# Performance work log

Measured on AMD Instinct MI355X. Metric: run time of the kernel, lower is better.

## Reference

```python
import jax, jax.numpy as jnp
import numpy as np

CHUNK = 32  # chunk_size in delta_rule_chunkwise


def _l2norm(x):
    return x * jax.lax.rsqrt(jnp.sum(x * x, axis=-1, keepdims=True) + 1e-6)


def setup_inputs() -> dict:
    key = jax.random.key(0)
    kq, kk, kv, kb = jax.random.split(key, 4)
    b, h, L, d = 4, 4, 8192, 128
    q = jax.random.normal(kq, (b, h, L, d), dtype=jnp.float32)
    k = jax.random.normal(kk, (b, h, L, d), dtype=jnp.float32)
    v = jax.random.normal(kv, (b, h, L, d), dtype=jnp.float32)
    beta = jax.random.uniform(kb, (b, h, L), dtype=jnp.float32)  # sigmoid(b_proj) in (0,1)
    return {"q": q, "k": k, "v": v, "beta": beta}


def reference(q, k, v, beta):
    """Chunkwise DeltaNet delta-rule: strictly causal, O(N) in seq length.
    q,k: [b,h,L,dk]; v: [b,h,L,dv]; beta: [b,h,L]. L must be a multiple of CHUNK.
    Returns (o [b,h,L,dv], final state S [b,h,dk,dv])."""
    b, h, L, dk = q.shape
    dv = v.shape[-1]
    c = CHUNK
    n = L // c

    qn = _l2norm(q)
    kn = _l2norm(k)
    vb = v * beta[..., None]
    kb = kn * beta[..., None]

    resh = lambda t: t.reshape(b, h, n, c, t.shape[-1])  # b h (n c) d -> b h n c d
    qc, kc, vc, kbc = map(resh, (qn, kn, vb, kb))

    # A = -(k_beta @ k^T) with upper triangle (incl diag) zeroed
    upper_incl = jnp.triu(jnp.ones((c, c), dtype=bool), 0)
    A = jnp.where(upper_incl, 0.0, -(kbc @ jnp.swapaxes(kc, -1, -2)))  # [b,h,n,c,c]

    # sequential forward substitution: inv[i,:i] += inv[i,:] @ inv[:,:i]
    col = jnp.arange(c)

    def row_body(i, inv):
        row = inv[..., i, :]                                   # [b,h,n,c]
        upd = row + jnp.einsum('...j,...jk->...k', row, inv)   # row @ inv
        return inv.at[..., i, :].set(jnp.where(col < i, upd, row))

    inv = jax.lax.fori_loop(1, c, row_body, A)
    inv = inv + jnp.eye(c, dtype=inv.dtype)

    u = inv @ vc    # [b,h,n,c,dv]
    w = inv @ kbc   # [b,h,n,c,dk]

    strict_upper = jnp.triu(jnp.ones((c, c), dtype=bool), 1)

    def step(S, xs):
        q_i, k_i, u_i0, w_i = xs                                   # [b,h,c,*]
        attn = jnp.where(strict_upper, 0.0, q_i @ jnp.swapaxes(k_i, -1, -2))
        u_i = u_i0 - w_i @ S
        o_i = q_i @ S + attn @ u_i
        S = S + jnp.swapaxes(k_i, -1, -2) @ u_i
        return S, o_i

    xs = tuple(jnp.moveaxis(t, 2, 0) for t in (qc, kc, u, w))      # [n,b,h,c,*]
    S0 = jnp.zeros((b, h, dk, dv), dtype=q.dtype)
    S, o = jax.lax.scan(step, S0, xs)
    o = jnp.moveaxis(o, 0, 2).reshape(b, h, L, dv)
    return o, S
```

## Files before the change

### kernel.cpp

```cpp
#include <hip/hip_runtime.h>


static constexpr int BH   = 16;
static constexpr int LQ   = 8192;
static constexpr int DK   = 128;
static constexpr int CC   = 32;
static constexpr int NCH  = LQ / CC;
static constexpr int LDP  = 132;
static constexpr int TP   = 36;

static constexpr size_t W_OFF  = 0;
static constexpr size_t U0_OFF = (size_t)BH * NCH * CC * DK;
static constexpr size_t AT_OFF = U0_OFF * 2;
static constexpr size_t RQ_OFF = AT_OFF + (size_t)BH * NCH * CC * CC;
static constexpr size_t RK_OFF = RQ_OFF + (size_t)BH * LQ;

__global__ __launch_bounds__(256) void dn_phase1(
    const float* __restrict__ q, const float* __restrict__ k,
    const float* __restrict__ v, const float* __restrict__ beta,
    float* __restrict__ ws)
{
    __shared__ float qc[CC][LDP];
    __shared__ float kc[CC][LDP];
    __shared__ float vc[CC][LDP];
    __shared__ float T[CC][TP];
    __shared__ float betas[CC], rqs[CC], rks[CC];

    const int tid = threadIdx.x;
    const int blk = blockIdx.x;
    const int bh  = blk >> 8;
    const int t   = blk & 255;
    const size_t gbase = ((size_t)bh * LQ + (size_t)t * CC) * DK;

    #pragma unroll
    for (int i = 0; i < 4; ++i) {
        int idx4 = i * 256 + tid;
        int row  = idx4 >> 5;
        int c4   = (idx4 & 31) << 2;
        *(float4*)&qc[row][c4] = *(const float4*)(q + gbase + (size_t)idx4 * 4);
        *(float4*)&kc[row][c4] = *(const float4*)(k + gbase + (size_t)idx4 * 4);
        *(float4*)&vc[row][c4] = *(const float4*)(v + gbase + (size_t)idx4 * 4);
    }
    if (tid < CC) betas[tid] = beta[(size_t)bh * LQ + (size_t)t * CC + tid];
    __syncthreads();

    {
        int row = tid >> 3, g = tid & 7;
        float sq = 0.f, sk = 0.f;
        #pragma unroll
        for (int i = 0; i < 4; ++i) {
            float4 a = *(float4*)&qc[row][g * 16 + i * 4];
            sq += a.x * a.x + a.y * a.y + a.z * a.z + a.w * a.w;
            float4 b = *(float4*)&kc[row][g * 16 + i * 4];
            sk += b.x * b.x + b.y * b.y + b.z * b.z + b.w * b.w;
        }
        sq += __shfl_xor(sq, 1); sq += __shfl_xor(sq, 2); sq += __shfl_xor(sq, 4);
        sk += __shfl_xor(sk, 1); sk += __shfl_xor(sk, 2); sk += __shfl_xor(sk, 4);
        if (g == 0) {
            rqs[row] = 1.f / sqrtf(sq + 1e-6f);
            rks[row] = 1.f / sqrtf(sk + 1e-6f);
        }
    }
    __syncthreads();

    if (tid < CC) {
        ws[RQ_OFF + (size_t)bh * LQ + (size_t)t * CC + tid] = rqs[tid];
        ws[RK_OFF + (size_t)bh * LQ + (size_t)t * CC + tid] = rks[tid];
    }

    #pragma unroll
    for (int i = 0; i < 4; ++i) {
        int idx4 = i * 256 + tid;
        int row  = idx4 >> 5;
        int c4   = (idx4 & 31) << 2;
        float rq_ = rqs[row], rk_ = rks[row];
        float4 a = *(float4*)&qc[row][c4];
        a.x *= rq_; a.y *= rq_; a.z *= rq_; a.w *= rq_;
        *(float4*)&qc[row][c4] = a;
        float4 b = *(float4*)&kc[row][c4];
        b.x *= rk_; b.y *= rk_; b.z *= rk_; b.w *= rk_;
        *(float4*)&kc[row][c4] = b;
    }
    __syncthreads();

    {
        int i  = tid >> 3;
        int j0 = (tid & 7) << 2;
        float aA[4] = {0.f, 0.f, 0.f, 0.f};
        float aQ[4] = {0.f, 0.f, 0.f, 0.f};
        for (int r4 = 0; r4 < 32; ++r4) {
            float4 ki = *(float4*)&kc[i][r4 << 2];
            float4 qi = *(float4*)&qc[i][r4 << 2];
            #pragma unroll
            for (int jj = 0; jj < 4; ++jj) {
                float4 kj = *(float4*)&kc[j0 + jj][r4 << 2];
                aA[jj] += ki.x * kj.x + ki.y * kj.y + ki.z * kj.z + ki.w * kj.w;
                aQ[jj] += qi.x * kj.x + qi.y * kj.y + qi.z * kj.z + qi.w * kj.w;
            }
        }
        float bi = betas[i];
        float at4[4];
        #pragma unroll
        for (int jj = 0; jj < 4; ++jj) {
            int j = j0 + jj;
            T[i][j] = (j < i) ? (-bi * aA[jj]) : 0.f;
            at4[jj] = (j <= i) ? aQ[jj] : 0.f;
        }
        *(float4*)(ws + AT_OFF + ((size_t)(bh * NCH + t) * CC + i) * CC + j0) =
            make_float4(at4[0], at4[1], at4[2], at4[3]);
    }
    __syncthreads();

    for (int i = 1; i < CC; ++i) {
        float upd = 0.f;
        if (tid < i) {
            float s = T[i][tid];
            for (int j = 0; j < CC; ++j) s += T[i][j] * T[j][tid];
            upd = s;
        }
        __syncthreads();
        if (tid < i) T[i][tid] = upd;
        __syncthreads();
    }

    {
        int i  = tid >> 3;
        int j0 = (tid & 7) << 2;
        #pragma unroll
        for (int jj = 0; jj < 4; ++jj) T[i][j0 + jj] *= betas[j0 + jj];
    }
    __syncthreads();

    {
        int i  = tid >> 3;
        int d0 = (tid & 7) << 4;
        float bi = betas[i];
        float4 aU[4], aW[4];
        #pragma unroll
        for (int d4 = 0; d4 < 4; ++d4) {
            float4 vv = *(float4*)&vc[i][d0 + d4 * 4];
            float4 kk = *(float4*)&kc[i][d0 + d4 * 4];
            aU[d4] = make_float4(bi * vv.x, bi * vv.y, bi * vv.z, bi * vv.w);
            aW[d4] = make_float4(bi * kk.x, bi * kk.y, bi * kk.z, bi * kk.w);
        }
        for (int j = 0; j < i; ++j) {
            float tb = T[i][j];
            #pragma unroll
            for (int d4 = 0; d4 < 4; ++d4) {
                float4 vv = *(float4*)&vc[j][d0 + d4 * 4];
                float4 kk = *(float4*)&kc[j][d0 + d4 * 4];
                aU[d4].x += tb * vv.x; aU[d4].y += tb * vv.y;
                aU[d4].z += tb * vv.z; aU[d4].w += tb * vv.w;
                aW[d4].x += tb * kk.x; aW[d4].y += tb * kk.y;
                aW[d4].z += tb * kk.z; aW[d4].w += tb * kk.w;
            }
        }
        size_t ob = (size_t)(bh * NCH + t) * (CC * DK) + (size_t)i * DK + d0;
        #pragma unroll
        for (int d4 = 0; d4 < 4; ++d4) {
            *(float4*)(ws + U0_OFF + ob + d4 * 4) = aU[d4];
            *(float4*)(ws + W_OFF  + ob + d4 * 4) = aW[d4];
        }
    }
}

__global__ __launch_bounds__(256) void dn_phase2(
    const float* __restrict__ q, const float* __restrict__ k,
    const float* __restrict__ ws, float* __restrict__ out)
{
    __shared__ float wA[CC][LDP], kA[CC][LDP], qA[CC][LDP];
    __shared__ float wB[CC][LDP], kB[CC][LDP], qB[CC][LDP];
    __shared__ float aA_[CC][TP], aB_[CC][TP];
    __shared__ float St[8][LDP];
    __shared__ float um_[CC][12];
    __shared__ float u2_[CC][12];

    const int bh  = blockIdx.x >> 4;
    const int g   = blockIdx.x & 15;
    const int c0  = g * 8;
    const int tid = threadIdx.x;
    const int a   = tid >> 3;
    const int c   = tid & 7;
    const int k2  = tid & 127;
    const int ch  = tid >> 7;

    float sreg0 = 0.f, sreg1 = 0.f, sreg2 = 0.f, sreg3 = 0.f;

    for (int idx = tid; idx < 8 * LDP; idx += 256) ((float*)St)[idx] = 0.f;

    float4 sw0, sw1, sw2, sw3, sk0, sk1, sk2_, sk3, sq0, sq1, sq2, sq3, sat;
    float nu0, nrq, nrk;

    auto issue = [&](int t) {
        const size_t wb = W_OFF + (size_t)(bh * NCH + t) * 4096;
        const size_t gb = ((size_t)bh * LQ + (size_t)t * CC) * DK;
        const size_t ab = AT_OFF + (size_t)(bh * NCH + t) * 1024;
        sw0 = *(const float4*)(ws + wb + (size_t)(0 * 256 + tid) * 4);
        sw1 = *(const float4*)(ws + wb + (size_t)(1 * 256 + tid) * 4);
        sw2 = *(const float4*)(ws + wb + (size_t)(2 * 256 + tid) * 4);
        sw3 = *(const float4*)(ws + wb + (size_t)(3 * 256 + tid) * 4);
        sk0 = *(const float4*)(k + gb + (size_t)(0 * 256 + tid) * 4);
        sk1 = *(const float4*)(k + gb + (size_t)(1 * 256 + tid) * 4);
        sk2_ = *(const float4*)(k + gb + (size_t)(2 * 256 + tid) * 4);
        sk3 = *(const float4*)(k + gb + (size_t)(3 * 256 + tid) * 4);
        sq0 = *(const float4*)(q + gb + (size_t)(0 * 256 + tid) * 4);
        sq1 = *(const float4*)(q + gb + (size_t)(1 * 256 + tid) * 4);
        sq2 = *(const float4*)(q + gb + (size_t)(2 * 256 + tid) * 4);
        sq3 = *(const float4*)(q + gb + (size_t)(3 * 256 + tid) * 4);
        sat = *(const float4*)(ws + ab + (size_t)tid * 4);
        nu0 = ws[U0_OFF + (size_t)(bh * NCH + t) * 4096 + (size_t)a * DK + c0 + c];
        nrq = ws[RQ_OFF + (size_t)bh * LQ + (size_t)t * CC + a];
        nrk = ws[RK_OFF + (size_t)bh * LQ + (size_t)t * CC + a];
    };

    auto commit = [&](float (*wT)[LDP], float (*kT)[LDP], float (*qT)[LDP],
                      float (*aT)[TP]) {
        {
            int gi = 0 * 256 + tid; int r = gi >> 5, c4 = (gi & 31) << 2;
            *(float4*)&wT[r][c4] = sw0; *(float4*)&kT[r][c4] = sk0; *(float4*)&qT[r][c4] = sq0;
        }
        {
            int gi = 1 * 256 + tid; int r = gi >> 5, c4 = (gi & 31) << 2;
            *(float4*)&wT[r][c4] = sw1; *(float4*)&kT[r][c4] = sk1; *(float4*)&qT[r][c4] = sq1;
        }
        {
            int gi = 2 * 256 + tid; int r = gi >> 5, c4 = (gi & 31) << 2;
            *(float4*)&wT[r][c4] = sw2; *(float4*)&kT[r][c4] = sk2_; *(float4*)&qT[r][c4] = sq2;
        }
        {
            int gi = 3 * 256 + tid; int r = gi >> 5, c4 = (gi & 31) << 2;
            *(float4*)&wT[r][c4] = sw3; *(float4*)&kT[r][c4] = sk3; *(float4*)&qT[r][c4] = sq3;
        }
        { int r = tid >> 3, c4 = (tid & 7) << 2; *(float4*)&aT[r][c4] = sat; }
    };

    float (*wC)[LDP] = wA, (*kC)[LDP] = kA, (*qC)[LDP] = qA;
    float (*wN)[LDP] = wB, (*kN)[LDP] = kB, (*qN)[LDP] = qB;
    float (*aC)[TP] = aA_, (*aN)[TP] = aB_;

    issue(0);
    commit(wC, kC, qC, aC);
    float u0r = nu0, rqr = nrq, rkr = nrk;
    __syncthreads();

    for (int t = 0; t < NCH; ++t) {
        if (t + 1 < NCH) issue(t + 1);

        float au = u0r, aq = 0.f;
        #pragma unroll
        for (int j = 0; j < 32; ++j) {
            float4 wv = *(float4*)&wC[a][4 * j];
            float4 qv = *(float4*)&qC[a][4 * j];
            float4 sv = *(float4*)&St[c][4 * j];
            au -= wv.x * sv.x + wv.y * sv.y + wv.z * sv.z + wv.w * sv.w;
            aq += qv.x * sv.x + qv.y * sv.y + qv.z * sv.z + qv.w * sv.w;
        }
        um_[a][c] = au;
        u2_[a][c] = au * rkr;
        float ao = rqr * aq;
        __syncthreads();

        #pragma unroll
        for (int j4 = 0; j4 < 8; ++j4) {
            float4 av = *(float4*)&aC[a][4 * j4];
            ao += av.x * um_[4 * j4 + 0][c] + av.y * um_[4 * j4 + 1][c]
                + av.z * um_[4 * j4 + 2][c] + av.w * um_[4 * j4 + 3][c];
        }
        out[((size_t)bh * LQ + (size_t)t * CC + a) * DK + c0 + c] = ao;

        #pragma unroll
        for (int jj = 0; jj < 32; ++jj) {
            float kv  = kC[jj][k2];
            float4 uv = *(float4*)&u2_[jj][4 * ch];
            sreg0 += kv * uv.x; sreg1 += kv * uv.y;
            sreg2 += kv * uv.z; sreg3 += kv * uv.w;
        }
        St[4 * ch + 0][k2] = sreg0;
        St[4 * ch + 1][k2] = sreg1;
        St[4 * ch + 2][k2] = sreg2;
        St[4 * ch + 3][k2] = sreg3;

        if (t + 1 < NCH) {
            commit(wN, kN, qN, aN);
            u0r = nu0; rqr = nrq; rkr = nrk;
            float (*tp)[LDP];
            tp = wC; wC = wN; wN = tp;
            tp = kC; kC = kN; kN = tp;
            tp = qC; qC = qN; qN = tp;
            float (*ta)[TP] = aC; aC = aN; aN = ta;
        }
        __syncthreads();
    }

    const size_t sbase = (size_t)BH * LQ * DK + (size_t)bh * DK * DK;
    *(float4*)(out + sbase + (size_t)k2 * DK + c0 + 4 * ch) =
        make_float4(sreg0, sreg1, sreg2, sreg3);
}

extern "C" void kernel_launch(void* const* d_in, const int* in_sizes, int n_in,
                              void* d_out, int out_size, void* d_ws, size_t ws_size,
                              hipStream_t stream) {
    (void)in_sizes; (void)n_in; (void)out_size; (void)ws_size;
    const float* q    = (const float*)d_in[0];
    const float* k    = (const float*)d_in[1];
    const float* v    = (const float*)d_in[2];
    const float* beta = (const float*)d_in[3];
    float* ws  = (float*)d_ws;
    float* out = (float*)d_out;

    dn_phase1<<<BH * NCH, 256, 0, stream>>>(q, k, v, beta, ws);
    dn_phase2<<<BH * 16, 256, 0, stream>>>(q, k, ws, out);
}
```

Before: 1.200 ms.

## Register-tile phase2 matmuls with split-K shuffle reductions for more reuse

Rewrites the per-chunk inner products in the sequential phase2 kernel. Each thread now computes a small register tile (2 rows x 4 columns) over a 16-wide slice of the inner dimension, and partial sums are combined with cross-lane shuffles. This raises data reuse per shared-memory load and shortens the serial dependency chains in the state update. W and Q are merged into a single shared buffer, and the Q contribution is staged through a new small array. The costs are extra shuffle reductions, idle lanes in some write phases, and higher register pressure under launch_bounds(256,1).

```diff
diff --git a/kernel.cpp b/kernel.cpp
--- a/kernel.cpp
+++ b/kernel.cpp
@@ -164,32 +164,44 @@
     }
 }
 
-__global__ __launch_bounds__(256) void dn_phase2(
+__global__ __launch_bounds__(256, 1) void dn_phase2(
     const float* __restrict__ q, const float* __restrict__ k,
     const float* __restrict__ ws, float* __restrict__ out)
 {
-    __shared__ float wA[CC][LDP], kA[CC][LDP], qA[CC][LDP];
-    __shared__ float wB[CC][LDP], kB[CC][LDP], qB[CC][LDP];
-    __shared__ float aA_[CC][TP], aB_[CC][TP];
+    __shared__ float wqA[64][LDP], wqB[64][LDP];
+    __shared__ float kA[CC][LDP],  kB[CC][LDP];
+    __shared__ float aA_[CC][TP],  aB_[CC][TP];
     __shared__ float St[8][LDP];
     __shared__ float um_[CC][12];
     __shared__ float u2_[CC][12];
-
-    const int bh  = blockIdx.x >> 4;
-    const int g   = blockIdx.x & 15;
-    const int c0  = g * 8;
-    const int tid = threadIdx.x;
-    const int a   = tid >> 3;
-    const int c   = tid & 7;
-    const int k2  = tid & 127;
-    const int ch  = tid >> 7;
-
-    float sreg0 = 0.f, sreg1 = 0.f, sreg2 = 0.f, sreg3 = 0.f;
-
-    for (int idx = tid; idx < 8 * LDP; idx += 256) ((float*)St)[idx] = 0.f;
-
-    float4 sw0, sw1, sw2, sw3, sk0, sk1, sk2_, sk3, sq0, sq1, sq2, sq3, sat;
-    float nu0, nrq, nrk;
+    __shared__ float qd_[CC][12];
+
+    const int bh   = blockIdx.x >> 4;
+    const int g    = blockIdx.x & 15;
+    const int c0   = g * 8;
+    const int tid  = threadIdx.x;
+    const int lane = tid & 63;
+    const int wv   = tid >> 6;
+
+    const int m4 = tid >> 4;
+    const int c2 = (tid >> 3) & 1;
+    const int ks = tid & 7;
+    const int a2  = tid >> 4;
+    const int cc_ = (tid >> 1) & 7;
+    const int jsC = tid & 1;
+    const int rlow = lane & 15;
+    const int chD  = (lane >> 4) & 1;
+    const int jsD  = lane >> 5;
+    const int rb   = 32 * wv + rlow;
+
+    float sreg0[4] = {0.f, 0.f, 0.f, 0.f};
+    float sreg1[4] = {0.f, 0.f, 0.f, 0.f};
+
+    float4 sw0, sw1, sw2, sw3, sq0, sq1, sq2, sq3, sk0, sk1, sk2_, sk3, sat;
+    float4 su0a, su0b;
+    float  srqa, srqb, srka, srkb;
+    float4 cu0a, cu0b;
+    float  crqa, crqb, crka, crkb;
 
     auto issue = [&](int t) {
         const size_t wb = W_OFF + (size_t)(bh * NCH + t) * 4096;
@@ -199,102 +211,179 @@
         sw1 = *(const float4*)(ws + wb + (size_t)(1 * 256 + tid) * 4);
         sw2 = *(const float4*)(ws + wb + (size_t)(2 * 256 + tid) * 4);
         sw3 = *(const float4*)(ws + wb + (size_t)(3 * 256 + tid) * 4);
+        sq0 = *(const float4*)(q + gb + (size_t)(0 * 256 + tid) * 4);
+        sq1 = *(const float4*)(q + gb + (size_t)(1 * 256 + tid) * 4);
+        sq2 = *(const float4*)(q + gb + (size_t)(2 * 256 + tid) * 4);
+        sq3 = *(const float4*)(q + gb + (size_t)(3 * 256 + tid) * 4);
         sk0 = *(const float4*)(k + gb + (size_t)(0 * 256 + tid) * 4);
         sk1 = *(const float4*)(k + gb + (size_t)(1 * 256 + tid) * 4);
         sk2_ = *(const float4*)(k + gb + (size_t)(2 * 256 + tid) * 4);
         sk3 = *(const float4*)(k + gb + (size_t)(3 * 256 + tid) * 4);
-        sq0 = *(const float4*)(q + gb + (size_t)(0 * 256 + tid) * 4);
-        sq1 = *(const float4*)(q + gb + (size_t)(1 * 256 + tid) * 4);
-        sq2 = *(const float4*)(q + gb + (size_t)(2 * 256 + tid) * 4);
-        sq3 = *(const float4*)(q + gb + (size_t)(3 * 256 + tid) * 4);
         sat = *(const float4*)(ws + ab + (size_t)tid * 4);
-        nu0 = ws[U0_OFF + (size_t)(bh * NCH + t) * 4096 + (size_t)a * DK + c0 + c];
-        nrq = ws[RQ_OFF + (size_t)bh * LQ + (size_t)t * CC + a];
-        nrk = ws[RK_OFF + (size_t)bh * LQ + (size_t)t * CC + a];
+        if (ks == 0) {
+            const size_t ub = U0_OFF + (size_t)(bh * NCH + t) * 4096;
+            su0a = *(const float4*)(ws + ub + (size_t)m4 * DK + c0 + 4 * c2);
+            su0b = *(const float4*)(ws + ub + (size_t)(m4 + 16) * DK + c0 + 4 * c2);
+            const size_t rbse = (size_t)bh * LQ + (size_t)t * CC;
+            srqa = ws[RQ_OFF + rbse + m4];
+            srqb = ws[RQ_OFF + rbse + m4 + 16];
+            srka = ws[RK_OFF + rbse + m4];
+            srkb = ws[RK_OFF + rbse + m4 + 16];
+        }
     };
 
-    auto commit = [&](float (*wT)[LDP], float (*kT)[LDP], float (*qT)[LDP],
-                      float (*aT)[TP]) {
+    auto commit = [&](float (*wqT)[LDP], float (*kT)[LDP], float (*aT)[TP]) {
         {
             int gi = 0 * 256 + tid; int r = gi >> 5, c4 = (gi & 31) << 2;
-            *(float4*)&wT[r][c4] = sw0; *(float4*)&kT[r][c4] = sk0; *(float4*)&qT[r][c4] = sq0;
+            *(float4*)&wqT[r][c4] = sw0; *(float4*)&wqT[32 + r][c4] = sq0;
+            *(float4*)&kT[r][c4] = sk0;
         }
         {
             int gi = 1 * 256 + tid; int r = gi >> 5, c4 = (gi & 31) << 2;
-            *(float4*)&wT[r][c4] = sw1; *(float4*)&kT[r][c4] = sk1; *(float4*)&qT[r][c4] = sq1;
+            *(float4*)&wqT[r][c4] = sw1; *(float4*)&wqT[32 + r][c4] = sq1;
+            *(float4*)&kT[r][c4] = sk1;
         }
         {
             int gi = 2 * 256 + tid; int r = gi >> 5, c4 = (gi & 31) << 2;
-            *(float4*)&wT[r][c4] = sw2; *(float4*)&kT[r][c4] = sk2_; *(float4*)&qT[r][c4] = sq2;
+            *(float4*)&wqT[r][c4] = sw2; *(float4*)&wqT[32 + r][c4] = sq2;
+            *(float4*)&kT[r][c4] = sk2_;
         }
         {
             int gi = 3 * 256 + tid; int r = gi >> 5, c4 = (gi & 31) << 2;
-            *(float4*)&wT[r][c4] = sw3; *(float4*)&kT[r][c4] = sk3; *(float4*)&qT[r][c4] = sq3;
+            *(float4*)&wqT[r][c4] = sw3; *(float4*)&wqT[32 + r][c4] = sq3;
+            *(float4*)&kT[r][c4] = sk3;
         }
         { int r = tid >> 3, c4 = (tid & 7) << 2; *(float4*)&aT[r][c4] = sat; }
     };
 
-    float (*wC)[LDP] = wA, (*kC)[LDP] = kA, (*qC)[LDP] = qA;
-    float (*wN)[LDP] = wB, (*kN)[LDP] = kB, (*qN)[LDP] = qB;
-    float (*aC)[TP] = aA_, (*aN)[TP] = aB_;
-
+    float (*wqC)[LDP] = wqA, (*wqN)[LDP] = wqB;
+    float (*kC)[LDP] = kA,  (*kN)[LDP] = kB;
+    float (*aC)[TP] = aA_,  (*aN)[TP] = aB_;
+
+    for (int idx = tid; idx < 8 * LDP; idx += 256) ((float*)St)[idx] = 0.f;
     issue(0);
-    commit(wC, kC, qC, aC);
-    float u0r = nu0, rqr = nrq, rkr = nrk;
+    commit(wqC, kC, aC);
+    cu0a = su0a; cu0b = su0b;
+    crqa = srqa; crqb = srqb; crka = srka; crkb = srkb;
     __syncthreads();
 
     for (int t = 0; t < NCH; ++t) {
         if (t + 1 < NCH) issue(t + 1);
 
-        float au = u0r, aq = 0.f;
-        #pragma unroll
-        for (int j = 0; j < 32; ++j) {
-            float4 wv = *(float4*)&wC[a][4 * j];
-            float4 qv = *(float4*)&qC[a][4 * j];
-            float4 sv = *(float4*)&St[c][4 * j];
-            au -= wv.x * sv.x + wv.y * sv.y + wv.z * sv.z + wv.w * sv.w;
-            aq += qv.x * sv.x + qv.y * sv.y + qv.z * sv.z + qv.w * sv.w;
-        }
-        um_[a][c] = au;
-        u2_[a][c] = au * rkr;
-        float ao = rqr * aq;
+        float accW0[4] = {0,0,0,0}, accW1[4] = {0,0,0,0};
+        float accQ0[4] = {0,0,0,0}, accQ1[4] = {0,0,0,0};
+        #pragma unroll
+        for (int it = 0; it < 4; ++it) {
+            const int kb = ks * 16 + it * 4;
+            float4 aw0 = *(float4*)&wqC[m4][kb];
+            float4 aw1 = *(float4*)&wqC[m4 + 16][kb];
+            float4 aq0 = *(float4*)&wqC[32 + m4][kb];
+            float4 aq1 = *(float4*)&wqC[48 + m4][kb];
+            #pragma unroll
+            for (int cc = 0; cc < 4; ++cc) {
+                float4 sv = *(float4*)&St[4 * c2 + cc][kb];
+                accW0[cc] += aw0.x * sv.x + aw0.y * sv.y + aw0.z * sv.z + aw0.w * sv.w;
+                accW1[cc] += aw1.x * sv.x + aw1.y * sv.y + aw1.z * sv.z + aw1.w * sv.w;
+                accQ0[cc] += aq0.x * sv.x + aq0.y * sv.y + aq0.z * sv.z + aq0.w * sv.w;
+                accQ1[cc] += aq1.x * sv.x + aq1.y * sv.y + aq1.z * sv.z + aq1.w * sv.w;
+            }
+        }
+        #pragma unroll
+        for (int m = 1; m <= 4; m <<= 1) {
+            #pragma unroll
+            for (int cc = 0; cc < 4; ++cc) {
+                accW0[cc] += __shfl_xor(accW0[cc], m);
+                accW1[cc] += __shfl_xor(accW1[cc], m);
+                accQ0[cc] += __shfl_xor(accQ0[cc], m);
+                accQ1[cc] += __shfl_xor(accQ1[cc], m);
+            }
+        }
+        if (ks == 0) {
+            float ua[4], ub[4];
+            ua[0] = cu0a.x - accW0[0]; ua[1] = cu0a.y - accW0[1];
+            ua[2] = cu0a.z - accW0[2]; ua[3] = cu0a.w - accW0[3];
+            ub[0] = cu0b.x - accW1[0]; ub[1] = cu0b.y - accW1[1];
+            ub[2] = cu0b.z - accW1[2]; ub[3] = cu0b.w - accW1[3];
+            *(float4*)&um_[m4][4 * c2]      = make_float4(ua[0], ua[1], ua[2], ua[3]);
+            *(float4*)&um_[m4 + 16][4 * c2] = make_float4(ub[0], ub[1], ub[2], ub[3]);
+            *(float4*)&u2_[m4][4 * c2] =
+                make_float4(ua[0] * crka, ua[1] * crka, ua[2] * crka, ua[3] * crka);
+            *(float4*)&u2_[m4 + 16][4 * c2] =
+                make_float4(ub[0] * crkb, ub[1] * crkb, ub[2] * crkb, ub[3] * crkb);
+            *(float4*)&qd_[m4][4 * c2] =
+                make_float4(accQ0[0] * crqa, accQ0[1] * crqa, accQ0[2] * crqa, accQ0[3] * crqa);
+            *(float4*)&qd_[m4 + 16][4 * c2] =
+                make_float4(accQ1[0] * crqb, accQ1[1] * crqb, accQ1[2] * crqb, accQ1[3] * crqb);
+        }
         __syncthreads();
 
-        #pragma unroll
-        for (int j4 = 0; j4 < 8; ++j4) {
-            float4 av = *(float4*)&aC[a][4 * j4];
-            ao += av.x * um_[4 * j4 + 0][c] + av.y * um_[4 * j4 + 1][c]
-                + av.z * um_[4 * j4 + 2][c] + av.w * um_[4 * j4 + 3][c];
-        }
-        out[((size_t)bh * LQ + (size_t)t * CC + a) * DK + c0 + c] = ao;
-
-        #pragma unroll
-        for (int jj = 0; jj < 32; ++jj) {
-            float kv  = kC[jj][k2];
-            float4 uv = *(float4*)&u2_[jj][4 * ch];
-            sreg0 += kv * uv.x; sreg1 += kv * uv.y;
-            sreg2 += kv * uv.z; sreg3 += kv * uv.w;
-        }
-        St[4 * ch + 0][k2] = sreg0;
-        St[4 * ch + 1][k2] = sreg1;
-        St[4 * ch + 2][k2] = sreg2;
-        St[4 * ch + 3][k2] = sreg3;
+        float oa = 0.f, ob = 0.f;
+        #pragma unroll
+        for (int jt = 0; jt < 4; ++jt) {
+            const int j = jsC * 16 + jt * 4;
+            float4 t0 = *(float4*)&aC[a2][j];
+            float4 t1 = *(float4*)&aC[a2 + 16][j];
+            float v0 = um_[j][cc_],     v1 = um_[j + 1][cc_];
+            float v2 = um_[j + 2][cc_], v3 = um_[j + 3][cc_];
+            oa += t0.x * v0 + t0.y * v1 + t0.z * v2 + t0.w * v3;
+            ob += t1.x * v0 + t1.y * v1 + t1.z * v2 + t1.w * v3;
+        }
+        oa += __shfl_xor(oa, 1);
+        ob += __shfl_xor(ob, 1);
+        if (jsC == 0) {
+            const size_t orow = (size_t)bh * LQ + (size_t)t * CC;
+            out[(orow + a2) * DK + c0 + cc_]      = oa + qd_[a2][cc_];
+            out[(orow + a2 + 16) * DK + c0 + cc_] = ob + qd_[a2 + 16][cc_];
+        }
+
+        float p0[4] = {0,0,0,0}, p1[4] = {0,0,0,0};
+        #pragma unroll
+        for (int jt = 0; jt < 4; ++jt) {
+            const int j = jsD * 16 + jt * 4;
+            #pragma unroll
+            for (int jj = 0; jj < 4; ++jj) {
+                float  kv0 = kC[j + jj][rb];
+                float  kv1 = kC[j + jj][rb + 16];
+                float4 uv  = *(float4*)&u2_[j + jj][4 * chD];
+                p0[0] += kv0 * uv.x; p0[1] += kv0 * uv.y;
+                p0[2] += kv0 * uv.z; p0[3] += kv0 * uv.w;
+                p1[0] += kv1 * uv.x; p1[1] += kv1 * uv.y;
+                p1[2] += kv1 * uv.z; p1[3] += kv1 * uv.w;
+            }
+        }
+        #pragma unroll
+        for (int i = 0; i < 4; ++i) {
+            p0[i] += __shfl_xor(p0[i], 32);
+            p1[i] += __shfl_xor(p1[i], 32);
+        }
+        if (jsD == 0) {
+            #pragma unroll
+            for (int i = 0; i < 4; ++i) { sreg0[i] += p0[i]; sreg1[i] += p1[i]; }
+            #pragma unroll
+            for (int cc = 0; cc < 4; ++cc) {
+                St[4 * chD + cc][rb]      = sreg0[cc];
+                St[4 * chD + cc][rb + 16] = sreg1[cc];
+            }
+        }
 
         if (t + 1 < NCH) {
-            commit(wN, kN, qN, aN);
-            u0r = nu0; rqr = nrq; rkr = nrk;
-            float (*tp)[LDP];
-            tp = wC; wC = wN; wN = tp;
-            tp = kC; kC = kN; kN = tp;
-            tp = qC; qC = qN; qN = tp;
-            float (*ta)[TP] = aC; aC = aN; aN = ta;
+            commit(wqN, kN, aN);
+            cu0a = su0a; cu0b = su0b;
+            crqa = srqa; crqb = srqb; crka = srka; crkb = srkb;
+            float (*tw)[LDP] = wqC; wqC = wqN; wqN = tw;
+            float (*tk)[LDP] = kC;  kC  = kN;  kN  = tk;
+            float (*ta)[TP]  = aC;  aC  = aN;  aN  = ta;
         }
         __syncthreads();
     }
 
-    const size_t sbase = (size_t)BH * LQ * DK + (size_t)bh * DK * DK;
-    *(float4*)(out + sbase + (size_t)k2 * DK + c0 + 4 * ch) =
-        make_float4(sreg0, sreg1, sreg2, sreg3);
+    if (jsD == 0) {
+        const size_t sbase = (size_t)BH * LQ * DK + (size_t)bh * DK * DK;
+        *(float4*)(out + sbase + (size_t)rb * DK + c0 + 4 * chD) =
+            make_float4(sreg0[0], sreg0[1], sreg0[2], sreg0[3]);
+        *(float4*)(out + sbase + (size_t)(rb + 16) * DK + c0 + 4 * chD) =
+            make_float4(sreg1[0], sreg1[1], sreg1[2], sreg1[3]);
+    }
 }
 
 extern "C" void kernel_launch(void* const* d_in, const int* in_sizes, int n_in,
```

Result: no change. 1.189 ms (-0.9%).
